# Kernel optimization log

Measured on AMD Instinct MI355X. Metric: run time of the kernel, lower is better.

Reference implementation:

```python
import jax, jax.numpy as jnp
import numpy as np

B, A, C, L, NH, SCALE = 1, 5, 64, 4, 8, 2
H = W = 24
S = 2 * C
KS = 5


def layernorm(x, g, b, eps=1e-5):
    m = x.mean(-1, keepdims=True)
    v = ((x - m) ** 2).mean(-1, keepdims=True)
    return (x - m) * jax.lax.rsqrt(v + eps) * g + b


def pe_1d(n, d):
    # PositionEncoding: temperature**(2*(i//2)/d), sin of even cols then cos of odd cols
    g = jnp.arange(d, dtype=jnp.float32)
    g = 10000.0 ** (2.0 * jnp.floor(g / 2.0) / d)
    p = jnp.arange(n, dtype=jnp.float32)[:, None] / g[None, :]
    return jnp.concatenate([jnp.sin(p[:, 0::2]), jnp.cos(p[:, 1::2])], axis=1)  # [n, d]


def mha(qk, v, in_w, out_w, nh, mask=None):
    # qk, v: [Lq, Bt, D]; torch nn.MultiheadAttention, bias-free, q=k=qk, value=v
    Lq, Bt, D = qk.shape
    dh = D // nh
    wq, wk, wv = jnp.split(in_w, 3, axis=0)
    q = (qk @ wq.T).reshape(Lq, Bt, nh, dh)
    k = (qk @ wk.T).reshape(Lq, Bt, nh, dh)
    vv = (v @ wv.T).reshape(Lq, Bt, nh, dh)
    s = jnp.einsum('lbhd,mbhd->bhlm', q, k) / jnp.sqrt(jnp.float32(dh))
    if mask is not None:
        s = s + mask
    a = jax.nn.softmax(s, axis=-1)
    o = jnp.einsum('bhlm,mbhd->lbhd', a, vv).reshape(Lq, Bt, D)
    return o @ out_w.T


def unfold3x3(x):
    # F.unfold(k=3, pad=1).permute(2,0,1): [N,c,h,w] -> [h*w, N, 9c] (c, kh, kw ordering)
    N, c, h, w = x.shape
    xp = jnp.pad(x, ((0, 0), (0, 0), (1, 1), (1, 1)))
    p = jnp.stack([xp[:, :, i:i + h, j:j + w] for i in range(3) for j in range(3)], axis=2)
    return p.reshape(N, c * 9, h * w).transpose(2, 0, 1)


def conv_hw(x5, w):
    # Conv3d kernel (1,3,3) pad (0,1,1): 2D conv per angular view
    Bc, Ci, Aa, h, w_ = x5.shape
    y = jax.lax.conv_general_dilated(
        x5.transpose(0, 2, 1, 3, 4).reshape(Bc * Aa, Ci, h, w_), w, (1, 1), ((1, 1), (1, 1)),
        dimension_numbers=('NCHW', 'OIHW', 'NCHW'))
    return y.reshape(Bc, Aa, w.shape[0], h, w_).transpose(0, 2, 1, 3, 4)


def window_mask(h, w, k):
    # SpaTrans.gen_mask: additive -inf outside a k x k local window
    kl, kr = k // 2, k - k // 2
    i = jnp.arange(h)
    j = jnp.arange(w)
    mh = (i[None, :] >= i[:, None] - kl) & (i[None, :] < i[:, None] + kr)
    mw = (j[None, :] >= j[:, None] - kl) & (j[None, :] < j[:, None] + kr)
    m = (mh[:, None, :, None] & mw[None, :, None, :]).reshape(h * w, h * w)
    return jnp.where(m, 0.0, -jnp.inf).astype(jnp.float32)


def setup_inputs() -> dict:
    key = jax.random.key(0)
    ks = iter(jax.random.split(key, 64))
    def nrm(shape, s=0.02):
        return jax.random.normal(next(ks), shape, dtype=jnp.float32) * s
    d = {}
    d['lr'] = jax.random.normal(next(ks), (B, 1, A * H, A * W), dtype=jnp.float32)
    Hh, Wh = H * SCALE, W * SCALE
    ch = -1.0 + (2.0 * jnp.arange(Hh, dtype=jnp.float32) + 1.0) / Hh
    cw = -1.0 + (2.0 * jnp.arange(Wh, dtype=jnp.float32) + 1.0) / Wh
    g = jnp.stack(jnp.meshgrid(ch, cw, indexing='ij'), axis=-1).reshape(-1, 2)
    d['coord'] = jnp.broadcast_to(g, (B, Hh * Wh, 2))
    d['conv0_w'] = nrm((C, 1, 3, 3), 0.1)
    d['convi_w'] = nrm((3, C, C, 3, 3), 0.05)
    d['ang_ln_g'] = jnp.ones((L, C)); d['ang_ln_b'] = jnp.zeros((L, C))
    d['ang_in'] = nrm((L, 3 * C, C)); d['ang_out'] = nrm((L, C, C))
    d['ang_ff_g'] = jnp.ones((L, C)); d['ang_ff_b'] = jnp.zeros((L, C))
    d['ang_w1'] = nrm((L, 2 * C, C)); d['ang_w2'] = nrm((L, C, 2 * C))
    d['spa_mlp'] = nrm((L, S, 9 * C))
    d['spa_ln_g'] = jnp.ones((L, S)); d['spa_ln_b'] = jnp.zeros((L, S))
    d['spa_in'] = nrm((L, 3 * S, S)); d['spa_out'] = nrm((L, S, S))
    d['spa_ff_g'] = jnp.ones((L, S)); d['spa_ff_b'] = jnp.zeros((L, S))
    d['spa_w1'] = nrm((L, 2 * S, S)); d['spa_w2'] = nrm((L, S, 2 * S))
    d['spa_lin'] = nrm((L, C, S))
    IN = A * A * C + 2 + 2 * A * A
    d['imp_w0'] = nrm((320, IN)); d['imp_b0'] = jnp.zeros((320,))
    d['imp_w1'] = nrm((320, 320)); d['imp_b1'] = jnp.zeros((320,))
    d['imp_w2'] = nrm((3 * A * A, 320)); d['imp_b2'] = jnp.zeros((3 * A * A,))
    return d


def reference(lr, coord, conv0_w, convi_w, ang_ln_g, ang_ln_b, ang_in, ang_out,
              ang_ff_g, ang_ff_b, ang_w1, ang_w2, spa_mlp, spa_ln_g, spa_ln_b,
              spa_in, spa_out, spa_ff_g, spa_ff_b, spa_w1, spa_w2, spa_lin,
              imp_w0, imp_b0, imp_w1, imp_b1, imp_w2, imp_b2):
    Bn = lr.shape[0]
    # 'b c (a1 h) (a2 w) -> b c (a1 a2) h w'
    x = lr.reshape(Bn, 1, A, H, A, W).transpose(0, 1, 2, 4, 3, 5).reshape(Bn, 1, A * A, H, W)
    spa_pe_img = ((pe_1d(H, C)[:, None, :] + pe_1d(W, C)[None, :, :]) * 0.5).transpose(2, 0, 1)[None]  # [1,C,h,w]
    ang_pe = pe_1d(A * A, C)[:, None, :]  # [A^2,1,C]
    buf = conv_hw(x, conv0_w)
    t = buf
    for i in range(3):
        t = jax.nn.leaky_relu(conv_hw(t, convi_w[i]), 0.2)
    buf = t + buf
    mask = window_mask(H, W, KS)
    blk = buf
    for l in range(L):
        # ---- AngTrans: tokens [A^2, B*h*w, C]
        tok = blk.transpose(2, 0, 3, 4, 1).reshape(A * A, Bn * H * W, C)
        tn = layernorm(tok + ang_pe, ang_ln_g[l], ang_ln_b[l])
        tok = mha(tn, tok, ang_in[l], ang_out[l], NH) + tok
        ff = layernorm(tok, ang_ff_g[l], ang_ff_b[l])
        tok = jax.nn.relu(ff @ ang_w1[l].T) @ ang_w2[l].T + tok
        blk = tok.reshape(A * A, Bn, H, W, C).transpose(1, 4, 0, 2, 3)
        # ---- SpaTrans: tokens [h*w, B*A^2, 2C] with local-window mask
        xb = blk.transpose(0, 2, 1, 3, 4).reshape(Bn * A * A, C, H, W)
        tok = unfold3x3(xb) @ spa_mlp[l].T
        pe_tok = unfold3x3(spa_pe_img) @ spa_mlp[l].T
        tn = layernorm(tok + pe_tok, spa_ln_g[l], spa_ln_b[l])
        tok = mha(tn, tok, spa_in[l], spa_out[l], NH, mask) + tok
        ff = layernorm(tok, spa_ff_g[l], spa_ff_b[l])
        tok = jax.nn.relu(ff @ spa_w1[l].T) @ spa_w2[l].T + tok
        t5 = tok.reshape(H, W, Bn, A * A, S).transpose(2, 4, 3, 0, 1)  # b s a h w
        blk = jnp.einsum('os,bsahw->boahw', spa_lin[l], t5)  # 1x1x1 Conv3d
    buf = blk + buf
    # 'b c (a1 a2) h w -> b c (a1 h) (a2 w)'
    feat_lr = buf.reshape(Bn, C, A, A, H, W).transpose(0, 1, 2, 4, 3, 5).reshape(Bn, C, A * H, A * W)
    Hh, Wh = H * SCALE, W * SCALE
    # per-view bilinear upsample (align_corners=False)
    v = feat_lr.reshape(Bn, C, A, H, A, W).transpose(0, 2, 4, 1, 3, 5).reshape(Bn * A * A, C, H, W)
    v = jax.image.resize(v, (Bn * A * A, C, Hh, Wh), method='bilinear')
    feat_hr = v.reshape(Bn, A, A, C, Hh, Wh).transpose(0, 4, 5, 1, 2, 3).reshape(Bn, Hh, Wh, A * A * C)
    # nearest grid_sample of LR cell-center coords -> relative coord
    c_ = jnp.clip(coord + 1e-6, -1 + 1e-6, 1 - 1e-6)
    ih = jnp.clip(jnp.round(((c_[..., 0] + 1) * H - 1) / 2), 0, H - 1)
    iw = jnp.clip(jnp.round(((c_[..., 1] + 1) * W - 1) / 2), 0, W - 1)
    qh = -1.0 + (2.0 * ih + 1.0) / H
    qw = -1.0 + (2.0 * iw + 1.0) / W
    rel = jnp.stack([(coord[..., 0] - qh) * H, (coord[..., 1] - qw) * W], axis=-1).reshape(Bn, Hh, Wh, 2)
    au = 0.5 + jnp.arange(A, dtype=jnp.float32)  # make_coord ranges [0,A]
    ca = jnp.stack(jnp.meshgrid(au, au, indexing='ij'), axis=-1).reshape(-1)
    ca = jnp.broadcast_to(ca, (Bn, Hh, Wh, 2 * A * A))
    inp = jnp.concatenate([feat_hr, rel, ca], axis=-1)
    h0 = jax.nn.relu(inp @ imp_w0.T + imp_b0)
    h1 = jax.nn.relu(h0 @ imp_w1.T + imp_b1)
    o = h1 @ imp_w2.T + imp_b2
    # 'b h w (a1 a2 c) -> b c (a1 h) (a2 w)', c=3
    return o.reshape(Bn, Hh, Wh, A, A, 3).transpose(0, 5, 3, 1, 4, 2).reshape(Bn, 3, A * Hh, A * Wh)
```

## Files before the change

### kernel.cpp

```cpp
#include <hip/hip_runtime.h>
#include <math.h>

typedef short  s16x4 __attribute__((ext_vector_type(4)));
typedef short  s16x8 __attribute__((ext_vector_type(8)));
typedef float  f32x4 __attribute__((ext_vector_type(4)));

static const size_t PE25_  = 0;
static const size_t SPAPE_ = 2048;
static const size_t X_     = 38912;
static const size_t CAV_   = 53312;
static const size_t PETOK_ = 54272;
static const size_t W9C_   = 349184;
static const size_t W9S_   = 459776;
static const size_t BUF_   = 754688;
static const size_t BLK_   = 1676288;
static const size_t ATOK_  = 2597888;
static const size_t TNF_   = 3519488;
static const size_t STOK_  = 4441088;
static const size_t STOK2_ = 6284288;
static const size_t AO_    = 8127488;
static const size_t QKV_   = 9970688;
static const size_t WS_FLOATS = 15500288;
static const size_t T0_ = QKV_ + 2764800;
static const size_t T1_ = T0_ + 921600;
static const size_t ZP_ = QKV_;
static const size_t H0_ = STOK_;
static const size_t H1_ = STOK2_;

__device__ inline ushort f2bf(float x) {
  unsigned u = __float_as_uint(x);
  u += 0x7fffu + ((u >> 16) & 1u);
  return (ushort)(u >> 16);
}
__device__ inline float bf2f(ushort h) { return __uint_as_float(((unsigned)h) << 16); }

__device__ inline void store_split(char* p, f32x4 v) {
  s16x4 hi, lo;
  #pragma unroll
  for (int e = 0; e < 4; ++e) {
    float x = v[e];
    ushort h = f2bf(x);
    ushort l = f2bf(x - bf2f(h));
    hi[e] = (short)h; lo[e] = (short)l;
  }
  *(s16x4*)p = hi;
  *(s16x4*)(p + 1024) = lo;
}

__device__ inline void scatter_split(char* base, int rr, int c6, float v) {
  ushort hi = f2bf(v);
  ushort lo = f2bf(v - bf2f(hi));
  int ks = c6 >> 5, kh = (c6 >> 4) & 1, k4 = (c6 >> 2) & 3;
  int lane2 = (k4 >> 1)*32 + ((rr & 15) << 1) + (k4 & 1);
  int byt = (((rr >> 4)*2 + ks) << 11) + (kh << 9) + (lane2 << 3) + (c6 & 3)*2;
  *(ushort*)(base + byt) = hi;
  *(ushort*)(base + byt + 1024) = lo;
}

__device__ inline void ld_bf16x16(const ushort* p, float* dst) {
  s16x8 a = *(const s16x8*)p;
  s16x8 b = *(const s16x8*)(p + 8);
  #pragma unroll
  for (int e = 0; e < 8; ++e) { dst[e] = bf2f((ushort)a[e]); dst[8 + e] = bf2f((ushort)b[e]); }
}

__device__ inline void slot_decode(int i, int wave, int lane,
                                   int& row, int& kof, int& wo) {
  int idx = (i << 2) + wave;
  int msub = idx >> 2, ks = (idx >> 1) & 1, kh = idx & 1;
  int rsub = (lane >> 1) & 15;
  int ksub = ((lane >> 5) << 3) + ((lane & 1) << 2);
  row = (msub << 4) + rsub;
  kof = (ks << 5) + (kh << 4) + ksub;
  wo = ((msub * 2 + ks) << 11) + (kh << 9) + (lane << 3);
}

__device__ inline void mfma_step(const char* ldsA, const char* ldsB, int lane,
                                 int wr, int wc, f32x4 acc[2][2]) {
  #pragma unroll
  for (int ks = 0; ks < 2; ++ks) {
    s16x8 ah[2], al[2], bh[2], bl[2];
    #pragma unroll
    for (int i = 0; i < 2; ++i) {
      const char* pa = ldsA + (((wr*2 + i)*2 + ks) << 11) + (lane << 4);
      ah[i] = *(const s16x8*)pa;
      al[i] = *(const s16x8*)(pa + 1024);
      const char* pb = ldsB + (((wc*2 + i)*2 + ks) << 11) + (lane << 4);
      bh[i] = *(const s16x8*)pb;
      bl[i] = *(const s16x8*)(pb + 1024);
    }
    #pragma unroll
    for (int i = 0; i < 2; ++i) {
      #pragma unroll
      for (int j = 0; j < 2; ++j) {
        acc[i][j] = __builtin_amdgcn_mfma_f32_16x16x32_bf16(ah[i], bh[j], acc[i][j], 0, 0, 0);
        acc[i][j] = __builtin_amdgcn_mfma_f32_16x16x32_bf16(ah[i], bl[j], acc[i][j], 0, 0, 0);
        acc[i][j] = __builtin_amdgcn_mfma_f32_16x16x32_bf16(al[i], bh[j], acc[i][j], 0, 0, 0);
      }
    }
  }
}

__device__ inline void epilogue(f32x4 acc[2][2], const float* bias, const float* res,
                                float* out, int N, int m0, int n0,
                                int wr, int wc, int lane, int act) {
  int colb = n0 + wc*32 + (lane & 15);
  int rowb = m0 + wr*32 + ((lane >> 4) << 2);
  #pragma unroll
  for (int j = 0; j < 2; ++j) {
    int cc = colb + j*16;
    if (cc >= N) continue;
    float bv = bias ? bias[cc] : 0.f;
    #pragma unroll
    for (int i = 0; i < 2; ++i) {
      #pragma unroll
      for (int r = 0; r < 4; ++r) {
        int rr = rowb + i*16 + r;
        float v = acc[i][j][r] + bv;
        if (act == 1) v = fmaxf(v, 0.f);
        else if (act == 2) v = v > 0.f ? v : 0.2f*v;
        if (res) v += res[(long)rr*N + cc];
        if (act == 3) {
          int hh = rr / 48, ww2 = rr % 48, q = cc / 3, ch = cc % 3;
          out[ch*57600 + ((q/5)*48 + hh)*240 + (q%5)*48 + ww2] = v;
        } else if (act == 4) {
          ((ushort*)out)[(long)rr*N + cc] = f2bf(v);
        } else {
          out[(long)rr*N + cc] = v;
        }
      }
    }
  }
}

template<int K, int LN>
__global__ __launch_bounds__(256) void mgemm3_k(
    const float* __restrict__ A, const float* __restrict__ A2, int nsplit,
    const float* __restrict__ pe, int pe_mode,
    const float* __restrict__ g, const float* __restrict__ bb,
    const float* __restrict__ W, const float* __restrict__ bias,
    const float* __restrict__ res, float* __restrict__ out,
    int N, int act, int Mreal, int Mpad) {
  constexpr int NCH = K / 64;
  __shared__ char Apl[NCH * 16384];
  __shared__ char Bp[16384];
  __shared__ float sw_[4][64][2];
  __shared__ float sf_[64][2];
  int bid = blockIdx.x;
  int m = bid % Mpad, nt = bid / Mpad;
  if (m >= Mreal) return;
  int m0 = m*64, n0 = nt*64;
  int t = threadIdx.x, lane = t & 63, wave = t >> 6;
  int wr = wave >> 1, wc = wave & 1;
  bool use_norm = LN && (n0 < nsplit);

  if (LN && use_norm) {
    f32x4 rv[NCH][4];
    float sA[4], sQ[4];
    #pragma unroll
    for (int i = 0; i < 4; ++i) { sA[i] = 0.f; sQ[i] = 0.f; }
    #pragma unroll
    for (int ch = 0; ch < NCH; ++ch)
      #pragma unroll
      for (int i = 0; i < 4; ++i) {
        int row, kof, wo;
        slot_decode(i, wave, lane, row, kof, wo);
        int gk = ch*64 + kof;
        f32x4 av = *(const f32x4*)&A[(long)(m0 + row)*K + gk];
        if (pe_mode == 0)      av += *(const f32x4*)&pe[(long)(m0/576)*K + gk];
        else if (pe_mode == 1) av += *(const f32x4*)&pe[(long)(m0%576 + row)*K + gk];
        rv[ch][i] = av;
        #pragma unroll
        for (int e = 0; e < 4; ++e) { sA[i] += av[e]; sQ[i] = fmaf(av[e], av[e], sQ[i]); }
      }
    #pragma unroll
    for (int i = 0; i < 4; ++i) {
      float s = sA[i], q = sQ[i];
      s += __shfl_xor(s, 1, 64);  q += __shfl_xor(q, 1, 64);
      s += __shfl_xor(s, 32, 64); q += __shfl_xor(q, 32, 64);
      if ((lane & 1) == 0 && lane < 32) {
        int row = i*16 + (lane >> 1);
        sw_[wave][row][0] = s; sw_[wave][row][1] = q;
      }
    }
    __syncthreads();
    if (t < 64) {
      float s = sw_[0][t][0] + sw_[1][t][0] + sw_[2][t][0] + sw_[3][t][0];
      float q = sw_[0][t][1] + sw_[1][t][1] + sw_[2][t][1] + sw_[3][t][1];
      float mean = s / K, var = q / K - mean*mean;
      sf_[t][0] = mean; sf_[t][1] = rsqrtf(var + 1e-5f);
    }
    __syncthreads();
    #pragma unroll
    for (int ch = 0; ch < NCH; ++ch)
      #pragma unroll
      for (int i = 0; i < 4; ++i) {
        int row, kof, wo;
        slot_decode(i, wave, lane, row, kof, wo);
        int gk = ch*64 + kof;
        float mean = sf_[row][0], rstd = sf_[row][1];
        f32x4 gv = *(const f32x4*)&g[gk];
        f32x4 bv = *(const f32x4*)&bb[gk];
        f32x4 nv;
        #pragma unroll
        for (int e = 0; e < 4; ++e) nv[e] = (rv[ch][i][e] - mean)*rstd*gv[e] + bv[e];
        store_split(Apl + ch*16384 + wo, nv);
      }
  } else {
    const float* As = LN ? A2 : A;
    #pragma unroll
    for (int ch = 0; ch < NCH; ++ch)
      #pragma unroll
      for (int i = 0; i < 4; ++i) {
        int row, kof, wo;
        slot_decode(i, wave, lane, row, kof, wo);
        f32x4 av = *(const f32x4*)&As[(long)(m0 + row)*K + ch*64 + kof];
        store_split(Apl + ch*16384 + wo, av);
      }
  }

  f32x4 pb[4];
  #pragma unroll
  for (int i = 0; i < 4; ++i) {
    int row, kof, wo;
    slot_decode(i, wave, lane, row, kof, wo);
    int br = n0 + row;
    pb[i] = (br < N) ? *(const f32x4*)&W[(long)br*K + kof] : (f32x4){0.f,0.f,0.f,0.f};
  }
  __syncthreads();
  f32x4 acc[2][2];
  #pragma unroll
  for (int i = 0; i < 2; ++i)
    #pragma unroll
    for (int j = 0; j < 2; ++j) acc[i][j] = (f32x4){0.f,0.f,0.f,0.f};
  for (int ch = 0; ch < NCH; ++ch) {
    #pragma unroll
    for (int i = 0; i < 4; ++i) {
      int row, kof, wo;
      slot_decode(i, wave, lane, row, kof, wo);
      store_split(Bp + wo, pb[i]);
    }
    __syncthreads();
    if (ch + 1 < NCH) {
      #pragma unroll
      for (int i = 0; i < 4; ++i) {
        int row, kof, wo;
        slot_decode(i, wave, lane, row, kof, wo);
        int br = n0 + row;
        pb[i] = (br < N) ? *(const f32x4*)&W[(long)br*K + (ch+1)*64 + kof]
                         : (f32x4){0.f,0.f,0.f,0.f};
      }
    }
    mfma_step(Apl + ch*16384, Bp, lane, wr, wc, acc);
    if (ch + 1 < NCH) __syncthreads();
  }
  epilogue(acc, bias, res, out, N, m0, n0, wr, wc, lane, act);
}

__global__ __launch_bounds__(256) void cgemm3_k(
    const float* __restrict__ in, const float* __restrict__ W9, long wstride,
    const float* __restrict__ res, float* __restrict__ out, long ostride,
    int N, int act, int Mreal, int Mpad) {
  __shared__ float halo[144 * 68];
  __shared__ char Ap[16384], Bp[16384];
  int bid = blockIdx.x;
  int m = bid % Mpad, nt = bid / Mpad;
  if (m >= Mreal) return;
  int ly = blockIdx.y;
  W9  += (long)ly * wstride;
  out += (long)ly * ostride;
  int m0 = m*64, n0 = nt*64;
  int a = m0 / 576, off = m0 % 576;
  int h_lo = off/24 - 1, h_hi = (off + 63)/24 + 1;
  int RH = h_hi - h_lo + 1;
  int t = threadIdx.x, lane = t & 63, wave = t >> 6;
  int wr = wave >> 1, wc = wave & 1;
  for (int sidx = t; sidx < RH*24*16; sidx += 256) {
    int tokr = sidx >> 4, c4 = (sidx & 15) << 2;
    int h = h_lo + tokr/24, w = tokr % 24;
    f32x4 v = {0.f,0.f,0.f,0.f};
    if ((unsigned)h < 24u) v = *(const f32x4*)&in[(long)(a*576 + h*24 + w)*64 + c4];
    *(f32x4*)&halo[tokr*68 + c4] = v;
  }
  f32x4 pb[4];
  #pragma unroll
  for (int i = 0; i < 4; ++i) {
    int row, kof, wo;
    slot_decode(i, wave, lane, row, kof, wo);
    int br = n0 + row;
    pb[i] = (br < N) ? *(const f32x4*)&W9[(long)br*64 + kof] : (f32x4){0.f,0.f,0.f,0.f};
  }
  __syncthreads();
  f32x4 acc[2][2];
  #pragma unroll
  for (int i = 0; i < 2; ++i)
    #pragma unroll
    for (int j = 0; j < 2; ++j) acc[i][j] = (f32x4){0.f,0.f,0.f,0.f};
  for (int ij = 0; ij < 9; ++ij) {
    int di = ij/3 - 1, dj = ij%3 - 1;
    #pragma unroll
    for (int i = 0; i < 4; ++i) {
      int row, kof, wo;
      slot_decode(i, wave, lane, row, kof, wo);
      int tok = off + row;
      int h2 = tok/24 + di, w2 = tok%24 + dj;
      f32x4 v = {0.f,0.f,0.f,0.f};
      if ((unsigned)h2 < 24u && (unsigned)w2 < 24u)
        v = *(const f32x4*)&halo[((h2 - h_lo)*24 + w2)*68 + kof];
      store_split(Ap + wo, v);
      store_split(Bp + wo, pb[i]);
    }
    __syncthreads();
    if (ij < 8) {
      #pragma unroll
      for (int i = 0; i < 4; ++i) {
        int row, kof, wo;
        slot_decode(i, wave, lane, row, kof, wo);
        int br = n0 + row;
        pb[i] = (br < N) ? *(const f32x4*)&W9[((long)(ij+1)*N + br)*64 + kof]
                         : (f32x4){0.f,0.f,0.f,0.f};
      }
    }
    mfma_step(Ap, Bp, lane, wr, wc, acc);
    if (ij < 8) __syncthreads();
  }
  epilogue(acc, nullptr, res, out, N, m0, n0, wr, wc, lane, act);
}

__global__ __launch_bounds__(256) void ang_mega_k(
    const ushort* __restrict__ qkv, const float* __restrict__ Wout,
    const float* __restrict__ blkr, const float* __restrict__ g,
    const float* __restrict__ bb, float* __restrict__ atok, float* __restrict__ tnf) {
  int hw = blockIdx.x;
  __shared__ float lq[25*192];
  __shared__ float lao[25*64];
  __shared__ float po[25*68];
  __shared__ float wout[64*65];
  __shared__ float st[25][2];
  int t = threadIdx.x;
  for (int idx = t; idx < 600; idx += 256) {
    int a3 = idx / 24, c8 = (idx % 24) * 8;
    s16x8 r = *(const s16x8*)&qkv[(long)(a3*576 + hw)*192 + c8];
    #pragma unroll
    for (int e = 0; e < 8; ++e) lq[a3*192 + c8 + e] = bf2f((ushort)r[e]);
  }
  for (int idx = t; idx < 4096; idx += 256) {
    int c = idx >> 6, d = idx & 63;
    wout[c*65 + d] = Wout[idx];
  }
  __syncthreads();
  if (t < 200) {
    int l = t / 8, head = t & 7;
    const float* q = lq + l*192 + head*8;
    float s[25]; float mx = -1e30f;
    #pragma unroll
    for (int mm = 0; mm < 25; ++mm) {
      const float* kk = lq + mm*192 + 64 + head*8;
      float acc = 0.f;
      #pragma unroll
      for (int d = 0; d < 8; ++d) acc = fmaf(q[d], kk[d], acc);
      acc *= 0.3535533905932738f;
      s[mm] = acc; mx = fmaxf(mx, acc);
    }
    float sum = 0.f;
    #pragma unroll
    for (int mm = 0; mm < 25; ++mm) { s[mm] = expf(s[mm] - mx); sum += s[mm]; }
    float inv = 1.f / sum;
    #pragma unroll
    for (int d = 0; d < 8; ++d) {
      float acc = 0.f;
      #pragma unroll
      for (int mm = 0; mm < 25; ++mm) acc = fmaf(s[mm], lq[mm*192 + 128 + head*8 + d], acc);
      lao[l*64 + head*8 + d] = acc * inv;
    }
  }
  __syncthreads();
  for (int idx = t; idx < 1600; idx += 256) {
    int tok = idx >> 6, c = idx & 63;
    const float* ar = &lao[tok*64];
    const float* wr = &wout[c*65];
    float accp = 0.f;
    #pragma unroll 16
    for (int d = 0; d < 64; ++d) accp = fmaf(ar[d], wr[d], accp);
    po[tok*68 + c] = accp + blkr[(long)(tok*576 + hw)*64 + c];
  }
  __syncthreads();
  if (t < 25) {
    float s = 0.f, q = 0.f;
    for (int c = 0; c < 64; ++c) { float x = po[t*68 + c]; s += x; q = fmaf(x, x, q); }
    float mean = s / 64.f, var = q / 64.f - mean*mean;
    st[t][0] = mean; st[t][1] = rsqrtf(var + 1e-5f);
  }
  __syncthreads();
  for (int idx = t; idx < 1600; idx += 256) {
    int tok = idx >> 6, c = idx & 63;
    float x = po[tok*68 + c];
    long gidx = (long)(tok*576 + hw)*64 + c;
    atok[gidx] = x;
    tnf[gidx] = (x - st[tok][0]) * st[tok][1] * g[c] + bb[c];
  }
}

__global__ __launch_bounds__(256) void ffn_ang_k(
    const float* __restrict__ tnf, const float* __restrict__ w1,
    const float* __restrict__ w2, float* __restrict__ atok,
    int Mreal, int Mpad) {
  __shared__ char Ap[16384], Bp[16384], Hp[2][16384];
  int bid = blockIdx.x;
  int m = bid % Mpad;
  if (m >= Mreal) return;
  int m0 = m*64;
  int t = threadIdx.x, lane = t & 63, wave = t >> 6;
  int wr = wave >> 1, wc = wave & 1;
  #pragma unroll
  for (int i = 0; i < 4; ++i) {
    int row, kof, wo;
    slot_decode(i, wave, lane, row, kof, wo);
    f32x4 av = *(const f32x4*)&tnf[(long)(m0 + row)*64 + kof];
    store_split(Ap + wo, av);
  }
  f32x4 pb[4];
  #pragma unroll
  for (int i = 0; i < 4; ++i) {
    int row, kof, wo;
    slot_decode(i, wave, lane, row, kof, wo);
    pb[i] = *(const f32x4*)&w1[(long)row*64 + kof];
  }
  __syncthreads();
  for (int nt = 0; nt < 2; ++nt) {
    #pragma unroll
    for (int i = 0; i < 4; ++i) {
      int row, kof, wo;
      slot_decode(i, wave, lane, row, kof, wo);
      store_split(Bp + wo, pb[i]);
    }
    __syncthreads();
    #pragma unroll
    for (int i = 0; i < 4; ++i) {
      int row, kof, wo;
      slot_decode(i, wave, lane, row, kof, wo);
      pb[i] = (nt == 0) ? *(const f32x4*)&w1[(long)(64 + row)*64 + kof]
                        : *(const f32x4*)&w2[(long)row*128 + kof];
    }
    f32x4 acc[2][2];
    #pragma unroll
    for (int i = 0; i < 2; ++i)
      #pragma unroll
      for (int j = 0; j < 2; ++j) acc[i][j] = (f32x4){0.f,0.f,0.f,0.f};
    mfma_step(Ap, Bp, lane, wr, wc, acc);
    #pragma unroll
    for (int jj = 0; jj < 2; ++jj)
      #pragma unroll
      for (int ii = 0; ii < 2; ++ii)
        #pragma unroll
        for (int r = 0; r < 4; ++r) {
          int rr = wr*32 + ii*16 + ((lane >> 4) << 2) + r;
          int cc = wc*32 + jj*16 + (lane & 15);
          scatter_split(Hp[nt], rr, cc, fmaxf(acc[ii][jj][r], 0.f));
        }
    __syncthreads();
  }
  f32x4 acc2[2][2];
  #pragma unroll
  for (int i = 0; i < 2; ++i)
    #pragma unroll
    for (int j = 0; j < 2; ++j) acc2[i][j] = (f32x4){0.f,0.f,0.f,0.f};
  for (int ch = 0; ch < 2; ++ch) {
    #pragma unroll
    for (int i = 0; i < 4; ++i) {
      int row, kof, wo;
      slot_decode(i, wave, lane, row, kof, wo);
      store_split(Bp + wo, pb[i]);
    }
    __syncthreads();
    if (ch == 0) {
      #pragma unroll
      for (int i = 0; i < 4; ++i) {
        int row, kof, wo;
        slot_decode(i, wave, lane, row, kof, wo);
        pb[i] = *(const f32x4*)&w2[(long)row*128 + 64 + kof];
      }
    }
    mfma_step(Hp[ch], Bp, lane, wr, wc, acc2);
    if (ch == 0) __syncthreads();
  }
  epilogue(acc2, nullptr, atok, atok, 64, m0, 0, wr, wc, lane, 0);
}

__global__ __launch_bounds__(512) void megaspa_k(
    const ushort* __restrict__ qkv, const float* __restrict__ stok,
    const float* __restrict__ wout, const float* __restrict__ g,
    const float* __restrict__ bb, const float* __restrict__ w1,
    const float* __restrict__ w2, const float* __restrict__ wlin,
    float* __restrict__ outb, int Mreal, int Mpad) {
  __shared__ char Aop[32768];
  __shared__ char SCR[65536];
  __shared__ float Rf[64*132];
  __shared__ float st[64][2];
  int bid = blockIdx.x;
  int m = bid % Mpad;
  if (m >= Mreal) return;
  int m0 = m*64;
  int t = threadIdx.x, lane = t & 63, wave = t >> 6;
  int wgrp = wave >> 2, w4 = wave & 3;
  int wr = w4 >> 1, wc = w4 & 1;
  char* Bp  = SCR + wgrp*16384;
  char* Hp0 = SCR + 32768;
  char* Hp1 = SCR + 49152;
  ushort* KV = (ushort*)SCR;

  for (int idx = t; idx < 2048; idx += 512) {
    int row = idx >> 5, c4 = (idx & 31) << 2;
    *(f32x4*)&Rf[row*132 + c4] = *(const f32x4*)&stok[(long)(m0 + row)*128 + c4];
  }

  int va = m0 / 576, off = m0 % 576;
  int hb = off/24 - 2;
  int he = (off + 63)/24 + 2;
  int RH = he - hb + 1;
  int rr1 = t >> 3, head = t & 7;
  int x = m0 + rr1;
  int hw = x % 576, h = hw / 24, w = hw % 24;
  float qr[16];
  ld_bf16x16(qkv + (long)x*384 + head*16, qr);
  for (int idx = t; idx < RH*24*16; idx += 512) {
    int tokr = idx >> 4, c8 = (idx & 15) << 3;
    int hh2 = hb + tokr/24, ww2 = tokr % 24;
    s16x8 vv = (s16x8){0,0,0,0,0,0,0,0};
    if ((unsigned)hh2 < 24u)
      vv = *(const s16x8*)&qkv[(long)(va*576 + hh2*24 + ww2)*384 + 128 + c8];
    *(s16x8*)&KV[tokr*136 + c8] = vv;
  }
  __syncthreads();
  float s[25]; float mx = -1e30f;
  #pragma unroll
  for (int ro = 0; ro < 5; ++ro) {
    int h2 = h + ro - 2;
    int hrow = h2 - hb;
    #pragma unroll
    for (int co = 0; co < 5; ++co) {
      int w2 = w + co - 2;
      int w2c = min(max(w2, 0), 23);
      const ushort* kp = &KV[(hrow*24 + w2c)*136 + head*16];
      s16x8 k0 = *(const s16x8*)kp;
      s16x8 k1 = *(const s16x8*)(kp + 8);
      float sc = -1e30f;
      if (h2 >= 0 && h2 < 24 && w2 >= 0 && w2 < 24) {
        sc = 0.f;
        #pragma unroll
        for (int d = 0; d < 8; ++d) sc = fmaf(qr[d], bf2f((ushort)k0[d]), sc);
        #pragma unroll
        for (int d = 0; d < 8; ++d) sc = fmaf(qr[8+d], bf2f((ushort)k1[d]), sc);
        sc *= 0.25f;
      }
      s[ro*5 + co] = sc; mx = fmaxf(mx, sc);
    }
  }
  float sum = 0.f;
  #pragma unroll
  for (int i = 0; i < 25; ++i) {
    float e = (s[i] > -1e29f) ? expf(s[i] - mx) : 0.f;
    s[i] = e; sum += e;
  }
  float inv = 1.f / sum;
  __syncthreads();
  for (int idx = t; idx < RH*24*16; idx += 512) {
    int tokr = idx >> 4, c8 = (idx & 15) << 3;
    int hh2 = hb + tokr/24, ww2 = tokr % 24;
    s16x8 vv = (s16x8){0,0,0,0,0,0,0,0};
    if ((unsigned)hh2 < 24u)
      vv = *(const s16x8*)&qkv[(long)(va*576 + hh2*24 + ww2)*384 + 256 + c8];
    *(s16x8*)&KV[tokr*136 + c8] = vv;
  }
  __syncthreads();
  {
    float acc[16];
    #pragma unroll
    for (int d = 0; d < 16; ++d) acc[d] = 0.f;
    #pragma unroll
    for (int ro = 0; ro < 5; ++ro) {
      int h2 = h + ro - 2;
      int hrow = h2 - hb;
      #pragma unroll
      for (int co = 0; co < 5; ++co) {
        int w2 = w + co - 2;
        int w2c = min(max(w2, 0), 23);
        const ushort* vp = &KV[(hrow*24 + w2c)*136 + head*16];
        s16x8 v0 = *(const s16x8*)vp;
        s16x8 v1 = *(const s16x8*)(vp + 8);
        float sv = s[ro*5 + co];
        #pragma unroll
        for (int d = 0; d < 8; ++d) acc[d] = fmaf(sv, bf2f((ushort)v0[d]), acc[d]);
        #pragma unroll
        for (int d = 0; d < 8; ++d) acc[8+d] = fmaf(sv, bf2f((ushort)v1[d]), acc[8+d]);
      }
    }
    #pragma unroll
    for (int d = 0; d < 16; ++d) {
      int cc = head*16 + d;
      scatter_split(Aop + (cc >> 6)*16384, rr1, cc & 63, acc[d] * inv);
    }
  }

  {
    int nt = wgrp;
    f32x4 acc[2][2];
    #pragma unroll
    for (int i = 0; i < 2; ++i)
      #pragma unroll
      for (int j = 0; j < 2; ++j) acc[i][j] = (f32x4){0.f,0.f,0.f,0.f};
    for (int ch = 0; ch < 2; ++ch) {
      __syncthreads();
      #pragma unroll
      for (int i = 0; i < 4; ++i) {
        int row, kof, wo;
        slot_decode(i, w4, lane, row, kof, wo);
        f32x4 bv = *(const f32x4*)&wout[(long)(nt*64 + row)*128 + ch*64 + kof];
        store_split(Bp + wo, bv);
      }
      __syncthreads();
      mfma_step(Aop + ch*16384, Bp, lane, wr, wc, acc);
    }
    int colb = nt*64 + wc*32 + (lane & 15);
    int rowb = wr*32 + ((lane >> 4) << 2);
    #pragma unroll
    for (int j = 0; j < 2; ++j)
      #pragma unroll
      for (int i = 0; i < 2; ++i)
        #pragma unroll
        for (int r = 0; r < 4; ++r) {
          int rr = rowb + i*16 + r, cc = colb + j*16;
          Rf[rr*132 + cc] += acc[i][j][r];
        }
  }
  __syncthreads();

  {
    int row = t >> 3, q8 = t & 7;
    const float* yr = &Rf[row*132 + q8*16];
    float sm = 0.f, sq = 0.f;
    #pragma unroll
    for (int j2 = 0; j2 < 16; ++j2) { float xv = yr[j2]; sm += xv; sq = fmaf(xv, xv, sq); }
    sm += __shfl_xor(sm, 1, 64); sq += __shfl_xor(sq, 1, 64);
    sm += __shfl_xor(sm, 2, 64); sq += __shfl_xor(sq, 2, 64);
    sm += __shfl_xor(sm, 4, 64); sq += __shfl_xor(sq, 4, 64);
    if (q8 == 0) {
      float mean = sm / 128.f, var = sq / 128.f - mean*mean;
      st[row][0] = mean; st[row][1] = rsqrtf(var + 1e-5f);
    }
  }
  __syncthreads();
  {
    int ch = wgrp;
    #pragma unroll
    for (int i = 0; i < 4; ++i) {
      int row, kof, wo;
      slot_decode(i, w4, lane, row, kof, wo);
      int gk = ch*64 + kof;
      f32x4 xv = *(const f32x4*)&Rf[row*132 + gk];
      float mean = st[row][0], rstd = st[row][1];
      f32x4 gv = *(const f32x4*)&g[gk];
      f32x4 bv = *(const f32x4*)&bb[gk];
      f32x4 nv;
      #pragma unroll
      for (int e = 0; e < 4; ++e) nv[e] = (xv[e] - mean)*rstd*gv[e] + bv[e];
      store_split(Aop + ch*16384 + wo, nv);
    }
  }

  f32x4 acc2[2][2];
  #pragma unroll
  for (int i = 0; i < 2; ++i)
    #pragma unroll
    for (int j = 0; j < 2; ++j) acc2[i][j] = (f32x4){0.f,0.f,0.f,0.f};
  for (int r = 0; r < 2; ++r) {
    int nt = 2*r + wgrp;
    f32x4 accH[2][2];
    #pragma unroll
    for (int i = 0; i < 2; ++i)
      #pragma unroll
      for (int j = 0; j < 2; ++j) accH[i][j] = (f32x4){0.f,0.f,0.f,0.f};
    for (int ch = 0; ch < 2; ++ch) {
      __syncthreads();
      #pragma unroll
      for (int i = 0; i < 4; ++i) {
        int row, kof, wo;
        slot_decode(i, w4, lane, row, kof, wo);
        f32x4 bv = *(const f32x4*)&w1[(long)(nt*64 + row)*128 + ch*64 + kof];
        store_split(Bp + wo, bv);
      }
      __syncthreads();
      mfma_step(Aop + ch*16384, Bp, lane, wr, wc, accH);
    }
    char* Hpw = wgrp ? Hp1 : Hp0;
    #pragma unroll
    for (int jj = 0; jj < 2; ++jj)
      #pragma unroll
      for (int ii = 0; ii < 2; ++ii)
        #pragma unroll
        for (int rx = 0; rx < 4; ++rx) {
          int rr = wr*32 + ii*16 + ((lane >> 4) << 2) + rx;
          int cc = wc*32 + jj*16 + (lane & 15);
          scatter_split(Hpw, rr, cc, fmaxf(accH[ii][jj][rx], 0.f));
        }
    for (int q = 0; q < 2; ++q) {
      __syncthreads();
      #pragma unroll
      for (int i = 0; i < 4; ++i) {
        int row, kof, wo;
        slot_decode(i, w4, lane, row, kof, wo);
        f32x4 bv = *(const f32x4*)&w2[(long)(wgrp*64 + row)*256 + (2*r + q)*64 + kof];
        store_split(Bp + wo, bv);
      }
      __syncthreads();
      mfma_step(q ? Hp1 : Hp0, Bp, lane, wr, wc, acc2);
    }
  }
  {
    int colb = wc*32 + (lane & 15);
    int rowb = wr*32 + ((lane >> 4) << 2);
    #pragma unroll
    for (int jj = 0; jj < 2; ++jj)
      #pragma unroll
      for (int ii = 0; ii < 2; ++ii)
        #pragma unroll
        for (int rx = 0; rx < 4; ++rx) {
          int rr = rowb + ii*16 + rx;
          int cc = colb + jj*16;
          scatter_split(Aop + wgrp*16384, rr, cc,
                        acc2[ii][jj][rx] + Rf[rr*132 + wgrp*64 + cc]);
        }
  }

  f32x4 acc3[2][2];
  #pragma unroll
  for (int i = 0; i < 2; ++i)
    #pragma unroll
    for (int j = 0; j < 2; ++j) acc3[i][j] = (f32x4){0.f,0.f,0.f,0.f};
  for (int ch = 0; ch < 2; ++ch) {
    __syncthreads();
    if (wgrp == 0) {
      #pragma unroll
      for (int i = 0; i < 4; ++i) {
        int row, kof, wo;
        slot_decode(i, w4, lane, row, kof, wo);
        f32x4 bv = *(const f32x4*)&wlin[(long)row*128 + ch*64 + kof];
        store_split(SCR + wo, bv);
      }
    }
    __syncthreads();
    if (wgrp == 0) mfma_step(Aop + ch*16384, SCR, lane, wr, wc, acc3);
  }
  if (wgrp == 0)
    epilogue(acc3, nullptr, nullptr, outb, 64, m0, 0, wr, wc, lane, 0);
}

__global__ __launch_bounds__(256) void zgemm3_k(
    const float* __restrict__ buf, const float* __restrict__ blk,
    const float* __restrict__ W0, float* __restrict__ Zp) {
  __shared__ char Ap[16384], Bp[16384];
  int bid = blockIdx.x;
  int m = bid % 9;
  int nz = bid / 9;
  int n = nz % 5, z = nz / 5;
  int m0 = m*64, n0 = n*64;
  int t = threadIdx.x, lane = t & 63, wave = t >> 6;
  int wr = wave >> 1, wc = wave & 1;
  f32x4 pa[4], pb[4];
  #pragma unroll
  for (int i = 0; i < 4; ++i) {
    int row, kof, wo;
    slot_decode(i, wave, lane, row, kof, wo);
    long tok = (long)(z*5)*576 + m0 + row;
    pa[i] = *(const f32x4*)&buf[tok*64 + kof];
    pa[i] += *(const f32x4*)&blk[tok*64 + kof];
    pb[i] = *(const f32x4*)&W0[(long)(n0 + row)*1652 + (z*5)*64 + kof];
  }
  f32x4 acc[2][2];
  #pragma unroll
  for (int i = 0; i < 2; ++i)
    #pragma unroll
    for (int j = 0; j < 2; ++j) acc[i][j] = (f32x4){0.f,0.f,0.f,0.f};
  for (int q = 0; q < 5; ++q) {
    #pragma unroll
    for (int i = 0; i < 4; ++i) {
      int row, kof, wo;
      slot_decode(i, wave, lane, row, kof, wo);
      store_split(Ap + wo, pa[i]);
      store_split(Bp + wo, pb[i]);
    }
    __syncthreads();
    if (q < 4) {
      #pragma unroll
      for (int i = 0; i < 4; ++i) {
        int row, kof, wo;
        slot_decode(i, wave, lane, row, kof, wo);
        long tok = (long)(z*5 + q + 1)*576 + m0 + row;
        pa[i] = *(const f32x4*)&buf[tok*64 + kof];
        pa[i] += *(const f32x4*)&blk[tok*64 + kof];
        pb[i] = *(const f32x4*)&W0[(long)(n0 + row)*1652 + (z*5 + q + 1)*64 + kof];
      }
    }
    mfma_step(Ap, Bp, lane, wr, wc, acc);
    if (q < 4) __syncthreads();
  }
  epilogue(acc, nullptr, nullptr, Zp + (long)z*184320, 320, m0, n0, wr, wc, lane, 0);
}

__global__ void combine_k(const float* __restrict__ Zp, const float* __restrict__ cav,
                          const float* __restrict__ coord, float* __restrict__ h0out) {
  int gidx = blockIdx.x * 256 + threadIdx.x;
  if (gidx >= 2304 * 320) return;
  int p = gidx / 320, o = gidx % 320;
  int hh = p / 48, ww = p % 48;
  float sh = hh * 0.5f - 0.25f, sw = ww * 0.5f - 0.25f;
  int h0i = (int)floorf(sh); float fh = sh - h0i;
  int w0i = (int)floorf(sw); float fw = sw - w0i;
  int h0c = max(h0i, 0), h1c = min(h0i + 1, 23);
  int w0c = max(w0i, 0), w1c = min(w0i + 1, 23);
  int i00 = (h0c*24 + w0c)*320 + o, i01 = (h0c*24 + w1c)*320 + o;
  int i10 = (h1c*24 + w0c)*320 + o, i11 = (h1c*24 + w1c)*320 + o;
  float z00 = 0.f, z01 = 0.f, z10 = 0.f, z11 = 0.f;
  #pragma unroll
  for (int z = 0; z < 5; ++z) {
    const float* Zz = Zp + (long)z*184320;
    z00 += Zz[i00]; z01 += Zz[i01]; z10 += Zz[i10]; z11 += Zz[i11];
  }
  float v = (1.f-fh)*((1.f-fw)*z00 + fw*z01) + fh*((1.f-fw)*z10 + fw*z11);
  #pragma unroll
  for (int d = 0; d < 2; ++d) {
    float co = coord[p*2 + d];
    float cc = fminf(fmaxf(co + 1e-6f, -1.f + 1e-6f), 1.f - 1e-6f);
    float ix = rintf(((cc + 1.f)*24.f - 1.f)*0.5f);
    ix = fminf(fmaxf(ix, 0.f), 23.f);
    float q = -1.f + (2.f*ix + 1.f)/24.f;
    v = fmaf((co - q)*24.f, cav[320*(d+1) + o], v);
  }
  h0out[gidx] = fmaxf(v + cav[o], 0.f);
}

__device__ inline float pe_val(int pos, int c) {
  int j = c & 31;
  float freq = powf(10000.f, -2.f * (float)j / 64.f);
  float arg = (float)pos * freq;
  return (c < 32) ? sinf(arg) : cosf(arg);
}

__global__ void setup_k(const float* __restrict__ lr, const float* __restrict__ convi_w,
                        const float* __restrict__ spa_mlp,
                        const float* __restrict__ imp_w0, const float* __restrict__ imp_b0,
                        float* pe25, float* spa_pe, float* X, float* w9c, float* w9s,
                        float* cav) {
  int g = blockIdx.x * 256 + threadIdx.x;
  if (g < 1600) { pe25[g] = pe_val(g >> 6, g & 63); return; }
  g -= 1600;
  if (g < 36864) {
    int hw = g >> 6, c = g & 63; int h = hw / 24, w = hw % 24;
    spa_pe[g] = 0.5f * (pe_val(h, c) + pe_val(w, c)); return;
  }
  g -= 36864;
  if (g < 14400) {
    int aa = g / 576, hw = g % 576, h = hw / 24, w = hw % 24;
    X[g] = lr[((aa/5)*24 + h)*120 + (aa%5)*24 + w]; return;
  }
  g -= 14400;
  if (g < 110592) {
    int cv = g / 36864, rem = g % 36864;
    int ij = rem / 4096, oc = rem % 4096;
    int o = oc >> 6, c = oc & 63;
    w9c[g] = convi_w[((long)(cv*64 + o)*64 + c)*9 + ij]; return;
  }
  g -= 110592;
  if (g < 294912) {
    int l = g / 73728, rem = g % 73728;
    int ij = rem / 8192, oc = rem % 8192;
    int o = oc >> 6, c = oc & 63;
    w9s[g] = spa_mlp[((long)(l*128 + o))*576 + c*9 + ij]; return;
  }
  g -= 294912;
  if (g < 320) {
    int o = g;
    float s = imp_b0[o];
    #pragma unroll
    for (int idx = 0; idx < 50; ++idx) {
      int pair = idx >> 1;
      float cvv = 0.5f + (float)((idx & 1) ? pair % 5 : pair / 5);
      s = fmaf(cvv, imp_w0[(long)o*1652 + 1602 + idx], s);
    }
    cav[o] = s;
    cav[320 + o] = imp_w0[(long)o*1652 + 1600];
    cav[640 + o] = imp_w0[(long)o*1652 + 1601];
  }
}

__global__ void conv0_k(const float* __restrict__ X, const float* __restrict__ W,
                        float* __restrict__ out) {
  int sp = threadIdx.x >> 6, lane = threadIdx.x & 63;
  int strip = blockIdx.x * 4 + sp;
  int a = strip / 48, r = strip % 48, h = r >> 1, w0 = (r & 1) * 12;
  __shared__ float patch[4][3][16];
  if (lane < 42) {
    int i = lane / 14, col = lane % 14;
    int h2 = h + i - 1, w2 = w0 + col - 1;
    float v = 0.f;
    if ((unsigned)h2 < 24u && (unsigned)w2 < 24u) v = X[a*576 + h2*24 + w2];
    patch[sp][i][col] = v;
  }
  __syncthreads();
  float wv[9];
  #pragma unroll
  for (int q = 0; q < 9; ++q) wv[q] = W[lane*9 + q];
  #pragma unroll
  for (int p = 0; p < 12; ++p) {
    float acc = 0.f;
    #pragma unroll
    for (int i = 0; i < 3; ++i)
      #pragma unroll
      for (int j = 0; j < 3; ++j)
        acc = fmaf(patch[sp][i][p + j], wv[i*3 + j], acc);
    out[(long)(a*576 + h*24 + w0 + p)*64 + lane] = acc;
  }
}

extern "C" void kernel_launch(void* const* d_in, const int* in_sizes, int n_in,
                              void* d_out, int out_size, void* d_ws, size_t ws_size,
                              hipStream_t stream) {
  (void)in_sizes; (void)n_in; (void)out_size;
  if (ws_size < (size_t)WS_FLOATS * 4) return;
  float* ws = (float*)d_ws;

  const float* lr       = (const float*)d_in[0];
  const float* coord    = (const float*)d_in[1];
  const float* conv0_w  = (const float*)d_in[2];
  const float* convi_w  = (const float*)d_in[3];
  const float* ang_ln_g = (const float*)d_in[4];
  const float* ang_ln_b = (const float*)d_in[5];
  const float* ang_in   = (const float*)d_in[6];
  const float* ang_out  = (const float*)d_in[7];
  const float* ang_ff_g = (const float*)d_in[8];
  const float* ang_ff_b = (const float*)d_in[9];
  const float* ang_w1   = (const float*)d_in[10];
  const float* ang_w2   = (const float*)d_in[11];
  const float* spa_mlp  = (const float*)d_in[12];
  const float* spa_ln_g = (const float*)d_in[13];
  const float* spa_ln_b = (const float*)d_in[14];
  const float* spa_in   = (const float*)d_in[15];
  const float* spa_out  = (const float*)d_in[16];
  const float* spa_ff_g = (const float*)d_in[17];
  const float* spa_ff_b = (const float*)d_in[18];
  const float* spa_w1   = (const float*)d_in[19];
  const float* spa_w2   = (const float*)d_in[20];
  const float* spa_lin  = (const float*)d_in[21];
  const float* imp_w0   = (const float*)d_in[22];
  const float* imp_b0   = (const float*)d_in[23];
  const float* imp_w1   = (const float*)d_in[24];
  const float* imp_b1   = (const float*)d_in[25];
  const float* imp_w2   = (const float*)d_in[26];
  const float* imp_b2   = (const float*)d_in[27];

  float* pe25 = ws + PE25_;  float* spa_pe = ws + SPAPE_;  float* X = ws + X_;
  float* cav = ws + CAV_;    float* petok = ws + PETOK_;
  float* w9c = ws + W9C_;    float* w9s = ws + W9S_;
  float* buf = ws + BUF_;    float* blk = ws + BLK_;      float* atok = ws + ATOK_;
  float* tnf = ws + TNF_;    float* stok = ws + STOK_;
  float* qkvf = ws + QKV_;   ushort* qkvh = (ushort*)(ws + QKV_);
  float* t0 = ws + T0_;      float* t1 = ws + T1_;
  float* Zp = ws + ZP_;      float* h0 = ws + H0_;        float* h1 = ws + H1_;

  setup_k<<<1792, 256, 0, stream>>>(lr, convi_w, spa_mlp, imp_w0, imp_b0,
                                    pe25, spa_pe, X, w9c, w9s, cav);
  conv0_k<<<300, 256, 0, stream>>>(X, conv0_w, buf);
  cgemm3_k<<<dim3(232,1), 256, 0, stream>>>(buf, w9c,         0, nullptr, t0,  0, 64, 2, 225, 232);
  cgemm3_k<<<dim3(232,1), 256, 0, stream>>>(t0,  w9c + 36864, 0, nullptr, t1,  0, 64, 2, 225, 232);
  cgemm3_k<<<dim3(232,1), 256, 0, stream>>>(t1,  w9c + 73728, 0, buf,     buf, 0, 64, 2, 225, 232);
  cgemm3_k<<<dim3(32, 4), 256, 0, stream>>>(spa_pe, w9s, 73728, nullptr, petok, 73728,
                                            128, 0, 9, 16);

  for (int l = 0; l < 4; ++l) {
    const float* blkr = (l == 0) ? buf : blk;
    mgemm3_k<64,1><<<696, 256, 0, stream>>>(blkr, blkr, 128, pe25, 0,
        ang_ln_g + l*64, ang_ln_b + l*64, ang_in + l*192*64, nullptr, nullptr,
        qkvf, 192, 4, 225, 232);
    ang_mega_k<<<576, 256, 0, stream>>>(qkvh, ang_out + l*64*64, blkr,
        ang_ff_g + l*64, ang_ff_b + l*64, atok, tnf);
    ffn_ang_k<<<232, 256, 0, stream>>>(tnf, ang_w1 + l*128*64, ang_w2 + l*64*128,
        atok, 225, 232);
    cgemm3_k<<<dim3(464,1), 256, 0, stream>>>(atok, w9s + l*73728, 0, nullptr, stok, 0,
        128, 0, 225, 232);
    mgemm3_k<128,1><<<1392, 256, 0, stream>>>(stok, stok, 256, petok + l*73728, 1,
        spa_ln_g + l*128, spa_ln_b + l*128, spa_in + l*384*128, nullptr, nullptr,
        qkvf, 384, 4, 225, 232);
    megaspa_k<<<232, 512, 0, stream>>>(qkvh, stok, spa_out + l*128*128,
        spa_ff_g + l*128, spa_ff_b + l*128, spa_w1 + l*256*128, spa_w2 + l*128*256,
        spa_lin + l*64*128, blk, 225, 232);
  }

  zgemm3_k<<<225, 256, 0, stream>>>(buf, blk, imp_w0, Zp);
  combine_k<<<2880, 256, 0, stream>>>(Zp, cav, coord, h0);
  mgemm3_k<320,0><<<200, 256, 0, stream>>>(h0, h0, 0, nullptr, -1, nullptr, nullptr,
      imp_w1, imp_b1, nullptr, h1, 320, 1, 36, 40);
  mgemm3_k<320,0><<<80, 256, 0, stream>>>(h1, h1, 0, nullptr, -1, nullptr, nullptr,
      imp_w2, imp_b2, nullptr, (float*)d_out, 75, 3, 36, 40);
}
```

Before: 601.9 us.

## Compute LayerNorm once per row tile and loop over QK N-tiles in QKV GEMM

Adds a new qkvg_k kernel that gives each block a 64-row M tile and loops over several N tiles. It normalizes the A tile with LayerNorm and positional encoding once, or loads V rows raw, then streams weight tiles through LDS and writes each N tile out in bf16. This removes the repeated per-N-tile LayerNorm and A-tile reload that mgemm3_k did, and launches fewer blocks. The cost is less parallelism (464 blocks instead of 696 or 1392) and serialized N-tile work inside each block.

```diff
diff --git a/kernel.cpp b/kernel.cpp
--- a/kernel.cpp
+++ b/kernel.cpp
@@ -18,7 +18,6 @@
 static const size_t TNF_   = 3519488;
 static const size_t STOK_  = 4441088;
 static const size_t STOK2_ = 6284288;
-static const size_t AO_    = 8127488;
 static const size_t QKV_   = 9970688;
 static const size_t WS_FLOATS = 15500288;
 static const size_t T0_ = QKV_ + 2764800;
@@ -133,6 +132,133 @@
   }
 }
 
+template<int K>
+__global__ __launch_bounds__(256) void qkvg_k(
+    const float* __restrict__ A, const float* __restrict__ pe, int pe_mode,
+    const float* __restrict__ g, const float* __restrict__ bb,
+    const float* __restrict__ W, float* __restrict__ out,
+    int NTr0, int NTr1, int N, int Mreal, int Mpad) {
+  constexpr int NCH = K / 64;
+  __shared__ char Apl[NCH * 16384];
+  __shared__ char Bp[16384];
+  __shared__ float sw_[4][64][2];
+  __shared__ float sf_[64][2];
+  int bid = blockIdx.x;
+  int type = bid / Mpad, m = bid % Mpad;
+  if (m >= Mreal) return;
+  int m0 = m*64;
+  int NTr = type ? NTr1 : NTr0;
+  int ntbase = type ? NTr0 : 0;
+  int t = threadIdx.x, lane = t & 63, wave = t >> 6;
+  int wr = wave >> 1, wc = wave & 1;
+
+  if (type == 0) {
+    f32x4 rv[NCH][4];
+    float sA[4], sQ[4];
+    #pragma unroll
+    for (int i = 0; i < 4; ++i) { sA[i] = 0.f; sQ[i] = 0.f; }
+    #pragma unroll
+    for (int ch = 0; ch < NCH; ++ch)
+      #pragma unroll
+      for (int i = 0; i < 4; ++i) {
+        int row, kof, wo;
+        slot_decode(i, wave, lane, row, kof, wo);
+        int gk = ch*64 + kof;
+        f32x4 av = *(const f32x4*)&A[(long)(m0 + row)*K + gk];
+        if (pe_mode == 0)      av += *(const f32x4*)&pe[(long)(m0/576)*K + gk];
+        else                   av += *(const f32x4*)&pe[(long)(m0%576 + row)*K + gk];
+        rv[ch][i] = av;
+        #pragma unroll
+        for (int e = 0; e < 4; ++e) { sA[i] += av[e]; sQ[i] = fmaf(av[e], av[e], sQ[i]); }
+      }
+    #pragma unroll
+    for (int i = 0; i < 4; ++i) {
+      float s = sA[i], q = sQ[i];
+      s += __shfl_xor(s, 1, 64);  q += __shfl_xor(q, 1, 64);
+      s += __shfl_xor(s, 32, 64); q += __shfl_xor(q, 32, 64);
+      if ((lane & 1) == 0 && lane < 32) {
+        int row = i*16 + (lane >> 1);
+        sw_[wave][row][0] = s; sw_[wave][row][1] = q;
+      }
+    }
+    __syncthreads();
+    if (t < 64) {
+      float s = sw_[0][t][0] + sw_[1][t][0] + sw_[2][t][0] + sw_[3][t][0];
+      float q = sw_[0][t][1] + sw_[1][t][1] + sw_[2][t][1] + sw_[3][t][1];
+      float mean = s / K, var = q / K - mean*mean;
+      sf_[t][0] = mean; sf_[t][1] = rsqrtf(var + 1e-5f);
+    }
+    __syncthreads();
+    #pragma unroll
+    for (int ch = 0; ch < NCH; ++ch)
+      #pragma unroll
+      for (int i = 0; i < 4; ++i) {
+        int row, kof, wo;
+        slot_decode(i, wave, lane, row, kof, wo);
+        int gk = ch*64 + kof;
+        float mean = sf_[row][0], rstd = sf_[row][1];
+        f32x4 gv = *(const f32x4*)&g[gk];
+        f32x4 bv = *(const f32x4*)&bb[gk];
+        f32x4 nv;
+        #pragma unroll
+        for (int e = 0; e < 4; ++e) nv[e] = (rv[ch][i][e] - mean)*rstd*gv[e] + bv[e];
+        store_split(Apl + ch*16384 + wo, nv);
+      }
+  } else {
+    #pragma unroll
+    for (int ch = 0; ch < NCH; ++ch)
+      #pragma unroll
+      for (int i = 0; i < 4; ++i) {
+        int row, kof, wo;
+        slot_decode(i, wave, lane, row, kof, wo);
+        f32x4 av = *(const f32x4*)&A[(long)(m0 + row)*K + ch*64 + kof];
+        store_split(Apl + ch*16384 + wo, av);
+      }
+  }
+
+  int S = NTr * NCH;
+  f32x4 pb[4];
+  #pragma unroll
+  for (int i = 0; i < 4; ++i) {
+    int row, kof, wo;
+    slot_decode(i, wave, lane, row, kof, wo);
+    pb[i] = *(const f32x4*)&W[(long)(ntbase*64 + row)*K + kof];
+  }
+  f32x4 acc[2][2];
+  #pragma unroll
+  for (int i = 0; i < 2; ++i)
+    #pragma unroll
+    for (int j = 0; j < 2; ++j) acc[i][j] = (f32x4){0.f,0.f,0.f,0.f};
+  for (int s = 0; s < S; ++s) {
+    int nt = s / NCH, ch = s % NCH;
+    __syncthreads();
+    #pragma unroll
+    for (int i = 0; i < 4; ++i) {
+      int row, kof, wo;
+      slot_decode(i, wave, lane, row, kof, wo);
+      store_split(Bp + wo, pb[i]);
+    }
+    __syncthreads();
+    if (s + 1 < S) {
+      int ntn = (s+1) / NCH, chn = (s+1) % NCH;
+      #pragma unroll
+      for (int i = 0; i < 4; ++i) {
+        int row, kof, wo;
+        slot_decode(i, wave, lane, row, kof, wo);
+        pb[i] = *(const f32x4*)&W[(long)((ntbase+ntn)*64 + row)*K + chn*64 + kof];
+      }
+    }
+    mfma_step(Apl + ch*16384, Bp, lane, wr, wc, acc);
+    if (ch == NCH - 1) {
+      epilogue(acc, nullptr, nullptr, out, N, m0, (ntbase+nt)*64, wr, wc, lane, 4);
+      #pragma unroll
+      for (int i = 0; i < 2; ++i)
+        #pragma unroll
+        for (int j = 0; j < 2; ++j) acc[i][j] = (f32x4){0.f,0.f,0.f,0.f};
+    }
+  }
+}
+
 template<int K, int LN>
 __global__ __launch_bounds__(256) void mgemm3_k(
     const float* __restrict__ A, const float* __restrict__ A2, int nsplit,
@@ -144,81 +270,22 @@
   constexpr int NCH = K / 64;
   __shared__ char Apl[NCH * 16384];
   __shared__ char Bp[16384];
-  __shared__ float sw_[4][64][2];
-  __shared__ float sf_[64][2];
   int bid = blockIdx.x;
   int m = bid % Mpad, nt = bid / Mpad;
   if (m >= Mreal) return;
   int m0 = m*64, n0 = nt*64;
   int t = threadIdx.x, lane = t & 63, wave = t >> 6;
   int wr = wave >> 1, wc = wave & 1;
-  bool use_norm = LN && (n0 < nsplit);
-
-  if (LN && use_norm) {
-    f32x4 rv[NCH][4];
-    float sA[4], sQ[4];
-    #pragma unroll
-    for (int i = 0; i < 4; ++i) { sA[i] = 0.f; sQ[i] = 0.f; }
-    #pragma unroll
-    for (int ch = 0; ch < NCH; ++ch)
-      #pragma unroll
-      for (int i = 0; i < 4; ++i) {
-        int row, kof, wo;
-        slot_decode(i, wave, lane, row, kof, wo);
-        int gk = ch*64 + kof;
-        f32x4 av = *(const f32x4*)&A[(long)(m0 + row)*K + gk];
-        if (pe_mode == 0)      av += *(const f32x4*)&pe[(long)(m0/576)*K + gk];
-        else if (pe_mode == 1) av += *(const f32x4*)&pe[(long)(m0%576 + row)*K + gk];
-        rv[ch][i] = av;
-        #pragma unroll
-        for (int e = 0; e < 4; ++e) { sA[i] += av[e]; sQ[i] = fmaf(av[e], av[e], sQ[i]); }
-      }
+  const float* As = LN ? A2 : A;
+  #pragma unroll
+  for (int ch = 0; ch < NCH; ++ch)
     #pragma unroll
     for (int i = 0; i < 4; ++i) {
-      float s = sA[i], q = sQ[i];
-      s += __shfl_xor(s, 1, 64);  q += __shfl_xor(q, 1, 64);
-      s += __shfl_xor(s, 32, 64); q += __shfl_xor(q, 32, 64);
-      if ((lane & 1) == 0 && lane < 32) {
-        int row = i*16 + (lane >> 1);
-        sw_[wave][row][0] = s; sw_[wave][row][1] = q;
-      }
-    }
-    __syncthreads();
-    if (t < 64) {
-      float s = sw_[0][t][0] + sw_[1][t][0] + sw_[2][t][0] + sw_[3][t][0];
-      float q = sw_[0][t][1] + sw_[1][t][1] + sw_[2][t][1] + sw_[3][t][1];
-      float mean = s / K, var = q / K - mean*mean;
-      sf_[t][0] = mean; sf_[t][1] = rsqrtf(var + 1e-5f);
-    }
-    __syncthreads();
-    #pragma unroll
-    for (int ch = 0; ch < NCH; ++ch)
-      #pragma unroll
-      for (int i = 0; i < 4; ++i) {
-        int row, kof, wo;
-        slot_decode(i, wave, lane, row, kof, wo);
-        int gk = ch*64 + kof;
-        float mean = sf_[row][0], rstd = sf_[row][1];
-        f32x4 gv = *(const f32x4*)&g[gk];
-        f32x4 bv = *(const f32x4*)&bb[gk];
-        f32x4 nv;
-        #pragma unroll
-        for (int e = 0; e < 4; ++e) nv[e] = (rv[ch][i][e] - mean)*rstd*gv[e] + bv[e];
-        store_split(Apl + ch*16384 + wo, nv);
-      }
-  } else {
-    const float* As = LN ? A2 : A;
-    #pragma unroll
-    for (int ch = 0; ch < NCH; ++ch)
-      #pragma unroll
-      for (int i = 0; i < 4; ++i) {
-        int row, kof, wo;
-        slot_decode(i, wave, lane, row, kof, wo);
-        f32x4 av = *(const f32x4*)&As[(long)(m0 + row)*K + ch*64 + kof];
-        store_split(Apl + ch*16384 + wo, av);
-      }
-  }
-
+      int row, kof, wo;
+      slot_decode(i, wave, lane, row, kof, wo);
+      f32x4 av = *(const f32x4*)&As[(long)(m0 + row)*K + ch*64 + kof];
+      store_split(Apl + ch*16384 + wo, av);
+    }
   f32x4 pb[4];
   #pragma unroll
   for (int i = 0; i < 4; ++i) {
@@ -581,6 +648,7 @@
     for (int ro = 0; ro < 5; ++ro) {
       int h2 = h + ro - 2;
       int hrow = h2 - hb;
+      (void)h2;
       #pragma unroll
       for (int co = 0; co < 5; ++co) {
         int w2 = w + co - 2;
@@ -978,18 +1046,18 @@
 
   for (int l = 0; l < 4; ++l) {
     const float* blkr = (l == 0) ? buf : blk;
-    mgemm3_k<64,1><<<696, 256, 0, stream>>>(blkr, blkr, 128, pe25, 0,
-        ang_ln_g + l*64, ang_ln_b + l*64, ang_in + l*192*64, nullptr, nullptr,
-        qkvf, 192, 4, 225, 232);
+    qkvg_k<64><<<464, 256, 0, stream>>>(blkr, pe25, 0,
+        ang_ln_g + l*64, ang_ln_b + l*64, ang_in + l*192*64, qkvf,
+        2, 1, 192, 225, 232);
     ang_mega_k<<<576, 256, 0, stream>>>(qkvh, ang_out + l*64*64, blkr,
         ang_ff_g + l*64, ang_ff_b + l*64, atok, tnf);
     ffn_ang_k<<<232, 256, 0, stream>>>(tnf, ang_w1 + l*128*64, ang_w2 + l*64*128,
         atok, 225, 232);
     cgemm3_k<<<dim3(464,1), 256, 0, stream>>>(atok, w9s + l*73728, 0, nullptr, stok, 0,
         128, 0, 225, 232);
-    mgemm3_k<128,1><<<1392, 256, 0, stream>>>(stok, stok, 256, petok + l*73728, 1,
-        spa_ln_g + l*128, spa_ln_b + l*128, spa_in + l*384*128, nullptr, nullptr,
-        qkvf, 384, 4, 225, 232);
+    qkvg_k<128><<<464, 256, 0, stream>>>(stok, petok + l*73728, 1,
+        spa_ln_g + l*128, spa_ln_b + l*128, spa_in + l*384*128, qkvf,
+        4, 2, 384, 225, 232);
     megaspa_k<<<232, 512, 0, stream>>>(qkvh, stok, spa_out + l*128*128,
         spa_ff_g + l*128, spa_ff_b + l*128, spa_w1 + l*256*128, spa_w2 + l*128*256,
         spa_lin + l*64*128, blk, 225, 232);
```

Result: faster. 558.2 us (-7.3%).
